# Performance work log

Measured on AMD Instinct MI355X. Metric: run time of the kernel, lower is better.

Reference implementation:

```python
import jax, jax.numpy as jnp
import numpy as np

LATENT_DIM = 64
CONTEXT_DIM = 128
NUM_LAYERS = 5
NUM_BINS = 8
HIDDEN = 256
TAIL_BOUND = 5.0
MIN_BIN_W = 1e-3
MIN_BIN_H = 1e-3
MIN_DERIV = 1e-3
BATCH = 32768


def setup_inputs() -> dict:
    key = jax.random.key(0)
    ks = jax.random.split(key, 8)
    D, C, L, H = LATENT_DIM, CONTEXT_DIM, NUM_LAYERS, HIDDEN
    out_dim = D * (3 * NUM_BINS - 1)  # 64*23 = 1472
    n_tri = D * (D - 1) // 2  # 2016
    s = 0.05
    return {
        "inputs": jax.random.normal(ks[0], (BATCH, D), jnp.float32) * 2.0,
        "context": jax.random.normal(ks[1], (BATCH, C), jnp.float32),
        "W1": jax.random.normal(ks[2], (L, C, H), jnp.float32) * s,
        "b1": jnp.zeros((L, H), jnp.float32),
        "W2": jax.random.normal(ks[3], (L, H, H), jnp.float32) * s,
        "b2": jnp.zeros((L, H), jnp.float32),
        "W3": jax.random.normal(ks[4], (L, H, out_dim), jnp.float32) * s,
        "b3": jnp.zeros((L, out_dim), jnp.float32),
        "lu_bias": jnp.zeros((L, D), jnp.float32),
        "lower_entries": jax.random.normal(ks[5], (L, n_tri), jnp.float32) * s,
        "upper_entries": jax.random.normal(ks[6], (L, n_tri), jnp.float32) * s,
        "upper_diag": jax.random.normal(ks[7], (L, D), jnp.float32) * s,
    }


def _unconstrained_rqs(x, uw, uh, ud):
    """Rational-quadratic spline with linear tails (nflows semantics).
    x: [B, D]; uw/uh: [B, D, NUM_BINS]; ud: [B, D, NUM_BINS-1].
    Returns (y [B,D], logabsdet [B,D])."""
    Bnd = TAIL_BOUND
    nb = NUM_BINS
    inside = (x >= -Bnd) & (x <= Bnd)
    # pad unnormalized derivatives so boundary derivative == 1
    const = float(np.log(np.exp(1.0 - MIN_DERIV) - 1.0))
    ud = jnp.pad(ud, ((0, 0), (0, 0), (1, 1)), constant_values=const)  # [B,D,nb+1]

    w = jax.nn.softmax(uw, axis=-1)
    w = MIN_BIN_W + (1.0 - MIN_BIN_W * nb) * w
    cumw = jnp.concatenate(
        [jnp.zeros(w.shape[:-1] + (1,), w.dtype), jnp.cumsum(w, axis=-1)], axis=-1)
    cumw = 2.0 * Bnd * cumw - Bnd
    cumw = cumw.at[..., 0].set(-Bnd).at[..., -1].set(Bnd)
    widths = cumw[..., 1:] - cumw[..., :-1]

    h = jax.nn.softmax(uh, axis=-1)
    h = MIN_BIN_H + (1.0 - MIN_BIN_H * nb) * h
    cumh = jnp.concatenate(
        [jnp.zeros(h.shape[:-1] + (1,), h.dtype), jnp.cumsum(h, axis=-1)], axis=-1)
    cumh = 2.0 * Bnd * cumh - Bnd
    cumh = cumh.at[..., 0].set(-Bnd).at[..., -1].set(Bnd)
    heights = cumh[..., 1:] - cumh[..., :-1]

    derivs = MIN_DERIV + jax.nn.softplus(ud)  # [B,D,nb+1]
    delta = heights / widths                  # [B,D,nb]

    xc = jnp.clip(x, -Bnd, Bnd)
    # searchsorted: sum(x >= bin_edges) - 1, clipped to valid bin range
    idx = jnp.clip(jnp.sum(xc[..., None] >= cumw, axis=-1) - 1, 0, nb - 1)[..., None]
    g = lambda a: jnp.take_along_axis(a, idx, axis=-1)[..., 0]

    in_cw = g(cumw)
    in_w = g(widths)
    in_ch = g(cumh)
    in_h = g(heights)
    in_delta = g(delta)
    in_d = g(derivs)
    in_d1 = g(derivs[..., 1:])

    theta = (xc - in_cw) / in_w
    tomt = theta * (1.0 - theta)
    numer = in_h * (in_delta * theta * theta + in_d * tomt)
    denom = in_delta + (in_d + in_d1 - 2.0 * in_delta) * tomt
    out = in_ch + numer / denom
    dnum = in_delta * in_delta * (
        in_d1 * theta * theta + 2.0 * in_delta * tomt + in_d * (1.0 - theta) ** 2)
    ld = jnp.log(dnum) - 2.0 * jnp.log(denom)

    return jnp.where(inside, out, x), jnp.where(inside, ld, 0.0)


def _lu_forward(x, lower_e, upper_e, udiag, bias):
    """nflows LULinear: y = L @ (U @ x) + b, logabsdet = sum(log diag(U))."""
    D = x.shape[-1]
    li = jnp.tril_indices(D, -1)
    ui = jnp.triu_indices(D, 1)
    Lm = jnp.eye(D, dtype=x.dtype).at[li].set(lower_e)
    diag = jax.nn.softplus(udiag) + 1e-3
    Um = jnp.zeros((D, D), x.dtype).at[ui].set(upper_e) + jnp.diag(diag)
    y = x @ Um.T
    y = y @ Lm.T + bias
    return y, jnp.sum(jnp.log(diag))


def reference(inputs, context, W1, b1, W2, b2, W3, b3,
              lu_bias, lower_entries, upper_entries, upper_diag):
    x = inputs
    logdet = jnp.zeros(x.shape[0], x.dtype)
    for l in range(NUM_LAYERS):
        # conditioning net (mask=ones => net sees only context)
        hh = jax.nn.relu(context @ W1[l] + b1[l])
        hh = jax.nn.relu(hh @ W2[l] + b2[l])
        params = (hh @ W3[l] + b3[l]).reshape(x.shape[0], LATENT_DIM, 3 * NUM_BINS - 1)
        uw = params[..., :NUM_BINS]
        uh = params[..., NUM_BINS:2 * NUM_BINS]
        ud = params[..., 2 * NUM_BINS:]
        x, ld = _unconstrained_rqs(x, uw, uh, ud)
        logdet = logdet + jnp.sum(ld, axis=-1)
        x, lld = _lu_forward(x, lower_entries[l], upper_entries[l],
                             upper_diag[l], lu_bias[l])
        logdet = logdet + lld
    base = -0.5 * jnp.sum(x * x, axis=-1) - 0.5 * LATENT_DIM * float(np.log(2.0 * np.pi))
    return base + logdet
```

## Files before the change

### kernel.cpp

```cpp
#include <hip/hip_runtime.h>
#include <hip/hip_bf16.h>
#include <math.h>

#define D 64
#define CDIM 128
#define NL 5
#define NB 8
#define HID 256
#define ODIM 1472
#define PPD 23
#define PPDP 24
#define NPAD 1536
#define NTRI 2016
#define BATCH 32768

#define FROWS 64
#define NCH 4
#define CPC 384
#define PPAD 392

typedef unsigned short u16;
typedef __attribute__((ext_vector_type(8))) short bf16x8;
typedef __attribute__((ext_vector_type(8))) unsigned short u16x8;
typedef __attribute__((ext_vector_type(4))) float f32x4;
typedef __attribute__((ext_vector_type(8))) float f32x8;

__device__ __forceinline__ float softplusf(float x) {
    return fmaxf(x, 0.0f) + log1pf(__expf(-fabsf(x)));
}
__device__ __forceinline__ float softplus_fast(float x) {
    return fmaxf(x, 0.0f) + __logf(1.0f + __expf(-fabsf(x)));
}
__device__ __forceinline__ float frcp(float x) { return __builtin_amdgcn_rcpf(x); }
__device__ __forceinline__ u16 f2bf(float f) {
    __hip_bfloat16 h = __float2bfloat16(f);
    return *reinterpret_cast<u16*>(&h);
}
__device__ __forceinline__ float bf2f(u16 u) {
    return __uint_as_float(((unsigned int)u) << 16);
}

__device__ __forceinline__ void gload16(const u16* g, const u16* s) {
    __builtin_amdgcn_global_load_lds(
        (const __attribute__((address_space(1))) unsigned int*)(unsigned long long)(uintptr_t)g,
        (__attribute__((address_space(3))) unsigned int*)(unsigned int)(uintptr_t)s,
        16, 0, 0);
}

__device__ __forceinline__ int xcd_swz(int bid, int nwg) {
    int q = nwg >> 3, r = nwg & 7;
    int xcd = bid & 7, idx = bid >> 3;
    return (xcd < r ? xcd * (q + 1) : r * (q + 1) + (xcd - r) * q) + idx;
}

__global__ void cvt_ctx(const float* __restrict__ c, u16* __restrict__ o) {
    int i = blockIdx.x * 256 + threadIdx.x;
    if (i < BATCH * CDIM) o[i] = f2bf(c[i]);
}

__global__ void prep_w12(const float* __restrict__ W1, const float* __restrict__ W2,
                         u16* __restrict__ W1t, u16* __restrict__ W2t) {
    int i = blockIdx.x * 256 + threadIdx.x;
    if (i < NL * HID * CDIM) {
        int k = i % CDIM; int n = (i / CDIM) % HID; int l = i / (CDIM * HID);
        W1t[i] = f2bf(W1[(l * CDIM + k) * HID + n]);
    }
    if (i < NL * HID * HID) {
        int k = i % HID; int n = (i / HID) % HID; int l = i / (HID * HID);
        W2t[i] = f2bf(W2[(l * HID + k) * HID + n]);
    }
}

__global__ void prep_w3(const float* __restrict__ W3, const float* __restrict__ b3,
                        u16* __restrict__ W3t, float* __restrict__ b3p) {
    int i = blockIdx.x * 256 + threadIdx.x;
    if (i < NL * NPAD * HID) {
        int k = i % HID; int n = (i / HID) % NPAD; int l = i / (HID * NPAD);
        int dd = n / PPDP, p = n % PPDP;
        W3t[i] = (p < PPD) ? f2bf(W3[(l * HID + k) * ODIM + dd * PPD + p]) : (u16)0;
    }
    if (i < NL * NPAD) {
        int n = i % NPAD; int l = i / NPAD;
        int dd = n / PPDP, p = n % PPDP;
        b3p[i] = (p < PPD) ? b3[l * ODIM + dd * PPD + p] : 0.0f;
    }
}

__global__ void lu_prep(const float* __restrict__ lower_e,
                        const float* __restrict__ upper_e,
                        const float* __restrict__ udiag,
                        float* __restrict__ At, float* __restrict__ lu_const) {
    int l = blockIdx.x;
    int t = threadIdx.x;
    __shared__ float Ls[D * D];
    __shared__ float Us[D * D];
    __shared__ float red[4];
    for (int idx = t; idx < D * D; idx += 256) {
        int i = idx >> 6, j = idx & 63;
        float lv;
        if (i == j)      lv = 1.0f;
        else if (i > j)  lv = lower_e[l * NTRI + (i * (i - 1)) / 2 + j];
        else             lv = 0.0f;
        Ls[idx] = lv;
        float uv;
        if (i == j)      uv = softplusf(udiag[l * D + i]) + 0.001f;
        else if (j > i)  uv = upper_e[l * NTRI + i * (D - 1) - (i * (i - 1)) / 2 + (j - i - 1)];
        else             uv = 0.0f;
        Us[idx] = uv;
    }
    __syncthreads();
    for (int idx = t; idx < D * D; idx += 256) {
        int i = idx >> 6, j = idx & 63;
        float acc = 0.0f;
        int km = min(i, j);
        for (int k = 0; k <= km; ++k) acc += Ls[i * D + k] * Us[k * D + j];
        At[(l * D + j) * D + i] = acc;
    }
    if (l == 0) {
        float s = 0.0f;
        for (int i = t; i < NL * D; i += 256)
            s += __logf(softplusf(udiag[i]) + 0.001f);
#pragma unroll
        for (int off = 32; off; off >>= 1) s += __shfl_xor(s, off);
        if ((t & 63) == 0) red[t >> 6] = s;
        __syncthreads();
        if (t == 0) lu_const[0] = red[0] + red[1] + red[2] + red[3];
    }
}

__global__ void init_kernel(const float* __restrict__ inp, float* __restrict__ x,
                            float* __restrict__ logdet) {
    int i = blockIdx.x * 256 + threadIdx.x;
    if (i < BATCH * D) x[i] = inp[i];
    if (i < BATCH) logdet[i] = 0.0f;
}

template<int RELU>
__global__ __launch_bounds__(256) void gemm_bf16(
    const u16* __restrict__ A0, const u16* __restrict__ Bt0,
    const float* __restrict__ bias0, u16* __restrict__ Cv0,
    int N, int K, int ncol, size_t sA, size_t sB, size_t sb, size_t sC)
{
    __shared__ u16 lds[16384];
    const int ly = blockIdx.y;
    const u16* A = A0 + (size_t)ly * sA;
    const u16* Bt = Bt0 + (size_t)ly * sB;
    const float* bias = bias0 + (size_t)ly * sb;
    u16* Cv = Cv0 + (size_t)ly * sC;
    const int t = threadIdx.x;
    const int w = t >> 6, l = t & 63;
    const int wm = w >> 1, wn = w & 1;
    const int wg = xcd_swz(blockIdx.x, gridDim.x);
    const size_t m0 = (size_t)(wg / ncol) * 128;
    const int n0 = (wg % ncol) * 128;
    const int lrow = l & 15, lk = l >> 4;
    const int srow = l >> 3, sslot = l & 7;

    f32x4 acc[4][4] = {};

    for (int k0 = 0; k0 < K; k0 += 64) {
#pragma unroll
        for (int q = 0; q < 4; ++q) {
            int c = q * 4 + w;
            int row = c * 8 + srow;
            int slog = sslot ^ (row & 7);
            gload16(A + (m0 + row) * K + k0 + slog * 8, &lds[c * 512]);
        }
#pragma unroll
        for (int q = 0; q < 4; ++q) {
            int c = q * 4 + w;
            int row = c * 8 + srow;
            int slog = sslot ^ (row & 7);
            gload16(Bt + (size_t)(n0 + row) * K + k0 + slog * 8, &lds[8192 + c * 512]);
        }
        __syncthreads();
#pragma unroll
        for (int ks = 0; ks < 2; ++ks) {
            bf16x8 a[4], b[4];
#pragma unroll
            for (int mf = 0; mf < 4; ++mf) {
                int row = wm * 64 + mf * 16 + lrow;
                int slot = (ks * 4 + lk) ^ (row & 7);
                a[mf] = *(const bf16x8*)&lds[row * 64 + slot * 8];
            }
#pragma unroll
            for (int nf = 0; nf < 4; ++nf) {
                int row = wn * 64 + nf * 16 + lrow;
                int slot = (ks * 4 + lk) ^ (row & 7);
                b[nf] = *(const bf16x8*)&lds[8192 + row * 64 + slot * 8];
            }
#pragma unroll
            for (int mf = 0; mf < 4; ++mf)
#pragma unroll
                for (int nf = 0; nf < 4; ++nf)
                    acc[mf][nf] = __builtin_amdgcn_mfma_f32_16x16x32_bf16(
                        a[mf], b[nf], acc[mf][nf], 0, 0, 0);
        }
        __syncthreads();
    }
#pragma unroll
    for (int nf = 0; nf < 4; ++nf) {
        int col = n0 + wn * 64 + nf * 16 + lrow;
        float bv = bias[col];
#pragma unroll
        for (int mf = 0; mf < 4; ++mf) {
            size_t rbase = m0 + wm * 64 + mf * 16 + lk * 4;
#pragma unroll
            for (int i = 0; i < 4; ++i) {
                float v = acc[mf][nf][i] + bv;
                if (RELU) v = fmaxf(v, 0.0f);
                Cv[(rbase + i) * N + col] = f2bf(v);
            }
        }
    }
}

__device__ __forceinline__ f32x8 cumb(f32x8 p) {
    float m = fmaxf(fmaxf(fmaxf(p[0], p[1]), fmaxf(p[2], p[3])),
                    fmaxf(fmaxf(p[4], p[5]), fmaxf(p[6], p[7])));
    f32x8 e;
    float s = 0.0f;
#pragma unroll
    for (int i = 0; i < 8; ++i) { e[i] = __expf(p[i] - m); s += e[i]; }
    float tt = 0.992f * frcp(s);
    f32x8 c;
    float run = 0.0f;
#pragma unroll
    for (int i = 0; i < 7; ++i) {
        run = fmaf(tt, e[i], run + 0.001f);
        c[i] = fmaf(10.0f, run, -5.0f);
    }
    c[7] = 5.0f;
    return c;
}

__device__ __forceinline__ void rqs_v(float xv, f32x8 uw, f32x8 uh, f32x8 ud,
                                      float& yo, float& ldo) {
    f32x8 cw = cumb(uw);
    f32x8 ch = cumb(uh);
    f32x8 dv;
#pragma unroll
    for (int i = 0; i < 7; ++i) dv[i] = 0.001f + softplus_fast(ud[i]);
    float xc = fminf(fmaxf(xv, -5.0f), 5.0f);
    float icw = -5.0f, icw1 = cw[0], ich = -5.0f, ich1 = ch[0];
    float d0 = 1.0f, d1 = dv[0];
#pragma unroll
    for (int k = 1; k < 8; ++k) {
        bool sel = (xc >= cw[k - 1]);
        icw  = sel ? cw[k - 1] : icw;
        icw1 = sel ? cw[k]     : icw1;
        ich  = sel ? ch[k - 1] : ich;
        ich1 = sel ? ch[k]     : ich1;
        d0   = sel ? dv[k - 1] : d0;
        d1   = sel ? ((k < 7) ? dv[k] : 1.0f) : d1;
    }
    float iw  = icw1 - icw;
    float ih  = ich1 - ich;
    float riw = frcp(iw);
    float dlt = ih * riw;
    float th  = (xc - icw) * riw;
    float omt = 1.0f - th;
    float tomt = th * omt;
    float numer = ih * (dlt * th * th + d0 * tomt);
    float den = dlt + (d0 + d1 - 2.0f * dlt) * tomt;
    float rden = frcp(den);
    float outv = ich + numer * rden;
    float dnum = dlt * dlt * (d1 * th * th + 2.0f * dlt * tomt + d0 * omt * omt);
    float ld = __logf(dnum * rden * rden);
    bool inside = (xv >= -5.0f) && (xv <= 5.0f);
    yo  = inside ? outv : xv;
    ldo = inside ? ld : 0.0f;
}

__global__ __launch_bounds__(512, 2) void gemm3_spline_lu(
    const u16* __restrict__ hh2,
    const u16* __restrict__ W3t,
    const float* __restrict__ b3p,
    const float* __restrict__ At, const float* __restrict__ lu_bias,
    float* __restrict__ x, float* __restrict__ logdet, int lay)
{
    __shared__ u16 hh2_s[FROWS * 256];
    __shared__ u16 params_s[FROWS * PPAD];
    __shared__ float y_s[FROWS * 65];
    __shared__ float ld_s[FROWS];
    const int t = threadIdx.x;
    const int w = t >> 6, ln = t & 63;
    const int lr = ln & 15, lk = ln >> 4;
    const int rbase = blockIdx.x * FROWS;

#pragma unroll
    for (int r = 0; r < 4; ++r) {
        int basec = (r * 8 + w) * 64;
        int c = basec + ln;
        int row = c >> 5, rem = c & 31;
        int kb = rem >> 3, sl = rem & 7;
        gload16(hh2 + (size_t)(rbase + row) * HID + kb * 64 + (sl ^ (row & 7)) * 8,
                &hh2_s[basec * 8]);
    }
    if (t < FROWS) ld_s[t] = 0.0f;
    __syncthreads();

    float ld_acc = 0.0f;
    const int srow = t & 63, sd0 = t >> 6;

    for (int ch = 0; ch < NCH; ++ch) {
        float xv0 = x[(size_t)(rbase + srow) * D + ch * 16 + sd0];
        float xv1 = x[(size_t)(rbase + srow) * D + ch * 16 + sd0 + 8];

        f32x4 acc[3][4] = {};
        const u16* wb = W3t + (size_t)(ch * CPC + w * 48 + lr) * HID + lk * 8;
#pragma unroll
        for (int ks = 0; ks < 8; ++ks) {
            bf16x8 hf[4];
#pragma unroll
            for (int rf = 0; rf < 4; ++rf) {
                int row = rf * 16 + lr;
                hf[rf] = *(const bf16x8*)&hh2_s[row * 256 + (ks >> 1) * 64
                              + ((((ks & 1) * 4) + lk) ^ (lr & 7)) * 8];
            }
#pragma unroll
            for (int mf = 0; mf < 3; ++mf) {
                bf16x8 wf = *(const bf16x8*)(wb + (size_t)mf * 16 * HID + ks * 32);
#pragma unroll
                for (int rf = 0; rf < 4; ++rf)
                    acc[mf][rf] = __builtin_amdgcn_mfma_f32_16x16x32_bf16(
                        wf, hf[rf], acc[mf][rf], 0, 0, 0);
            }
        }
        __syncthreads();

        {
            const float* bb = b3p + ch * CPC + w * 48 + 4 * lk;
#pragma unroll
            for (int mf = 0; mf < 3; ++mf) {
                float4 bv = *(const float4*)(bb + mf * 16);
#pragma unroll
                for (int rf = 0; rf < 4; ++rf) {
                    f32x4 v = acc[mf][rf];
                    unsigned int lo = (unsigned int)f2bf(v[0] + bv.x)
                                    | ((unsigned int)f2bf(v[1] + bv.y) << 16);
                    unsigned int hi = (unsigned int)f2bf(v[2] + bv.z)
                                    | ((unsigned int)f2bf(v[3] + bv.w) << 16);
                    uint2 pv; pv.x = lo; pv.y = hi;
                    int r = rf * 16 + lr;
                    int cbase = w * 48 + mf * 16 + 4 * lk;
                    *(uint2*)&params_s[r * PPAD + cbase] = pv;
                }
            }
        }
        __syncthreads();

#pragma unroll
        for (int pr = 0; pr < 2; ++pr) {
            int dg = ch * 16 + sd0 + pr * 8;
            const u16x8* pp = (const u16x8*)&params_s[srow * PPAD + (sd0 + pr * 8) * PPDP];
            u16x8 q0 = pp[0], q1 = pp[1], q2 = pp[2];
            f32x8 uw, uh, ud;
#pragma unroll
            for (int j = 0; j < 8; ++j) {
                uw[j] = bf2f(q0[j]);
                uh[j] = bf2f(q1[j]);
                ud[j] = bf2f(q2[j]);
            }
            float xv = pr ? xv1 : xv0;
            float y, ldv;
            rqs_v(xv, uw, uh, ud, y, ldv);
            y_s[srow * 65 + dg] = y;
            ld_acc += ldv;
        }
    }

    atomicAdd(&ld_s[srow], ld_acc);
    __syncthreads();
    if (t < FROWS) logdet[rbase + t] += ld_s[t];

#pragma unroll
    for (int p = 0; p < 8; ++p) {
        int idx = p * 512 + t;
        int r = idx >> 6, i = idx & 63;
        float acc2 = lu_bias[lay * D + i];
        const float* ap = At + (size_t)lay * D * D + i;
#pragma unroll 8
        for (int j = 0; j < D; ++j)
            acc2 = fmaf(y_s[r * 65 + j], ap[j * D], acc2);
        x[(size_t)(rbase + r) * D + i] = acc2;
    }
}

__global__ void final_kernel(const float* __restrict__ x,
                             const float* __restrict__ logdet,
                             const float* __restrict__ lu_const,
                             float* __restrict__ out) {
    int t = threadIdx.x;
    int b = blockIdx.x * 4 + (t >> 6);
    int d = t & 63;
    float v = x[(size_t)b * D + d];
    float s = v * v;
#pragma unroll
    for (int off = 32; off; off >>= 1) s += __shfl_xor(s, off);
    if (d == 0)
        out[b] = logdet[b] + lu_const[0] - 0.5f * s - 0.5f * 64.0f * 1.8378770664093453f;
}

extern "C" void kernel_launch(void* const* d_in, const int* in_sizes, int n_in,
                              void* d_out, int out_size, void* d_ws, size_t ws_size,
                              hipStream_t stream) {
    const float* inputs  = (const float*)d_in[0];
    const float* context = (const float*)d_in[1];
    const float* W1      = (const float*)d_in[2];
    const float* b1      = (const float*)d_in[3];
    const float* W2      = (const float*)d_in[4];
    const float* b2      = (const float*)d_in[5];
    const float* W3      = (const float*)d_in[6];
    const float* b3      = (const float*)d_in[7];
    const float* lu_bias = (const float*)d_in[8];
    const float* lower_e = (const float*)d_in[9];
    const float* upper_e = (const float*)d_in[10];
    const float* udiag   = (const float*)d_in[11];
    float* out = (float*)d_out;

    char* p = (char*)d_ws;
    auto alloc = [&](size_t bytes) { void* r = p; p += (bytes + 255) & ~(size_t)255; return r; };
    float* x        = (float*)alloc((size_t)BATCH * D * 4);
    float* logdet   = (float*)alloc((size_t)BATCH * 4);
    float* At       = (float*)alloc((size_t)NL * D * D * 4);
    float* lu_const = (float*)alloc(256);
    u16*   ctx_bf   = (u16*)alloc((size_t)BATCH * CDIM * 2);
    u16*   hh1      = (u16*)alloc((size_t)NL * BATCH * HID * 2);
    u16*   hh2      = (u16*)alloc((size_t)NL * BATCH * HID * 2);
    u16*   W1t      = (u16*)alloc((size_t)NL * HID * CDIM * 2);
    u16*   W2t      = (u16*)alloc((size_t)NL * HID * HID * 2);
    u16*   W3t      = (u16*)alloc((size_t)NL * NPAD * HID * 2);
    float* b3p      = (float*)alloc((size_t)NL * NPAD * 4);

    cvt_ctx<<<(BATCH * CDIM + 255) / 256, 256, 0, stream>>>(context, ctx_bf);
    prep_w12<<<(NL * HID * HID + 255) / 256, 256, 0, stream>>>(W1, W2, W1t, W2t);
    prep_w3<<<(NL * NPAD * HID + 255) / 256, 256, 0, stream>>>(W3, b3, W3t, b3p);
    lu_prep<<<NL, 256, 0, stream>>>(lower_e, upper_e, udiag, At, lu_const);
    init_kernel<<<(BATCH * D + 255) / 256, 256, 0, stream>>>(inputs, x, logdet);

    dim3 gmlp((BATCH / 128) * 2, NL);
    gemm_bf16<1><<<gmlp, 256, 0, stream>>>(
        ctx_bf, W1t, b1, hh1, HID, CDIM, 2,
        0, (size_t)HID * CDIM, HID, (size_t)BATCH * HID);
    gemm_bf16<1><<<gmlp, 256, 0, stream>>>(
        hh1, W2t, b2, hh2, HID, HID, 2,
        (size_t)BATCH * HID, (size_t)HID * HID, HID, (size_t)BATCH * HID);

    for (int lay = 0; lay < NL; ++lay) {
        gemm3_spline_lu<<<BATCH / FROWS, 512, 0, stream>>>(
            hh2 + (size_t)lay * BATCH * HID,
            W3t + (size_t)lay * NPAD * HID, b3p + (size_t)lay * NPAD,
            At, lu_bias, x, logdet, lay);
    }
    final_kernel<<<BATCH / 4, 256, 0, stream>>>(x, logdet, lu_const, out);
}
```

Before: 588.0 us.

## Split GEMM3 into smaller chunks, raise occupancy, swizzle params LDS, reuse LU weights

Halves the per-chunk output width (8 chunks of 192 columns) and splits the 8 waves as 4 column groups by 2 row groups, so each wave holds a 3x2 accumulator set instead of 3x4. This cuts register pressure and allows launch bounds of 4 blocks per CU. The params LDS buffer shrinks and uses an XOR swizzle instead of padding to avoid bank conflicts. The LU matvec now reuses each At element across 8 rows per thread. The costs are more chunk iterations and barriers, plus lower MFMA reuse of the loaded W3 fragments.

```diff
diff --git a/kernel.cpp b/kernel.cpp
--- a/kernel.cpp
+++ b/kernel.cpp
@@ -15,9 +15,9 @@
 #define BATCH 32768
 
 #define FROWS 64
-#define NCH 4
-#define CPC 384
-#define PPAD 392
+#define NCH 8
+#define CPC 192
+#define PROWB 384
 
 typedef unsigned short u16;
 typedef __attribute__((ext_vector_type(8))) short bf16x8;
@@ -272,7 +272,7 @@
     ldo = inside ? ld : 0.0f;
 }
 
-__global__ __launch_bounds__(512, 2) void gemm3_spline_lu(
+__global__ __launch_bounds__(512, 4) void gemm3_spline_lu(
     const u16* __restrict__ hh2,
     const u16* __restrict__ W3t,
     const float* __restrict__ b3p,
@@ -280,12 +280,13 @@
     float* __restrict__ x, float* __restrict__ logdet, int lay)
 {
     __shared__ u16 hh2_s[FROWS * 256];
-    __shared__ u16 params_s[FROWS * PPAD];
+    __shared__ u16 params_s[FROWS * CPC];
     __shared__ float y_s[FROWS * 65];
     __shared__ float ld_s[FROWS];
     const int t = threadIdx.x;
     const int w = t >> 6, ln = t & 63;
     const int lr = ln & 15, lk = ln >> 4;
+    const int wc = w & 3, wr = w >> 2;
     const int rbase = blockIdx.x * FROWS;
 
 #pragma unroll
@@ -301,20 +302,19 @@
     __syncthreads();
 
     float ld_acc = 0.0f;
-    const int srow = t & 63, sd0 = t >> 6;
+    const int srow = ln, sd = w;
 
     for (int ch = 0; ch < NCH; ++ch) {
-        float xv0 = x[(size_t)(rbase + srow) * D + ch * 16 + sd0];
-        float xv1 = x[(size_t)(rbase + srow) * D + ch * 16 + sd0 + 8];
-
-        f32x4 acc[3][4] = {};
-        const u16* wb = W3t + (size_t)(ch * CPC + w * 48 + lr) * HID + lk * 8;
+        float xv = x[(size_t)(rbase + srow) * D + ch * 8 + sd];
+
+        f32x4 acc[3][2] = {};
+        const u16* wb = W3t + (size_t)(ch * CPC + wc * 48 + lr) * HID + lk * 8;
 #pragma unroll
         for (int ks = 0; ks < 8; ++ks) {
-            bf16x8 hf[4];
-#pragma unroll
-            for (int rf = 0; rf < 4; ++rf) {
-                int row = rf * 16 + lr;
+            bf16x8 hf[2];
+#pragma unroll
+            for (int rf = 0; rf < 2; ++rf) {
+                int row = wr * 32 + rf * 16 + lr;
                 hf[rf] = *(const bf16x8*)&hh2_s[row * 256 + (ks >> 1) * 64
                               + ((((ks & 1) * 4) + lk) ^ (lr & 7)) * 8];
             }
@@ -322,7 +322,7 @@
             for (int mf = 0; mf < 3; ++mf) {
                 bf16x8 wf = *(const bf16x8*)(wb + (size_t)mf * 16 * HID + ks * 32);
 #pragma unroll
-                for (int rf = 0; rf < 4; ++rf)
+                for (int rf = 0; rf < 2; ++rf)
                     acc[mf][rf] = __builtin_amdgcn_mfma_f32_16x16x32_bf16(
                         wf, hf[rf], acc[mf][rf], 0, 0, 0);
             }
@@ -330,31 +330,33 @@
         __syncthreads();
 
         {
-            const float* bb = b3p + ch * CPC + w * 48 + 4 * lk;
+            const float* bb = b3p + ch * CPC + wc * 48 + 4 * lk;
 #pragma unroll
             for (int mf = 0; mf < 3; ++mf) {
                 float4 bv = *(const float4*)(bb + mf * 16);
 #pragma unroll
-                for (int rf = 0; rf < 4; ++rf) {
+                for (int rf = 0; rf < 2; ++rf) {
                     f32x4 v = acc[mf][rf];
                     unsigned int lo = (unsigned int)f2bf(v[0] + bv.x)
                                     | ((unsigned int)f2bf(v[1] + bv.y) << 16);
                     unsigned int hi = (unsigned int)f2bf(v[2] + bv.z)
                                     | ((unsigned int)f2bf(v[3] + bv.w) << 16);
                     uint2 pv; pv.x = lo; pv.y = hi;
-                    int r = rf * 16 + lr;
-                    int cbase = w * 48 + mf * 16 + 4 * lk;
-                    *(uint2*)&params_s[r * PPAD + cbase] = pv;
+                    int r = wr * 32 + rf * 16 + lr;
+                    int slot = wc * 6 + mf * 2 + (lk >> 1);
+                    int boff = r * PROWB + (((slot ^ (r & 7)) << 4) | ((lk & 1) << 3));
+                    *(uint2*)((char*)params_s + boff) = pv;
                 }
             }
         }
         __syncthreads();
 
-#pragma unroll
-        for (int pr = 0; pr < 2; ++pr) {
-            int dg = ch * 16 + sd0 + pr * 8;
-            const u16x8* pp = (const u16x8*)&params_s[srow * PPAD + (sd0 + pr * 8) * PPDP];
-            u16x8 q0 = pp[0], q1 = pp[1], q2 = pp[2];
+        {
+            int base = srow * PROWB;
+            int s0 = 3 * sd, rx = srow & 7;
+            u16x8 q0 = *(const u16x8*)((const char*)params_s + base + (((s0 + 0) ^ rx) << 4));
+            u16x8 q1 = *(const u16x8*)((const char*)params_s + base + (((s0 + 1) ^ rx) << 4));
+            u16x8 q2 = *(const u16x8*)((const char*)params_s + base + (((s0 + 2) ^ rx) << 4));
             f32x8 uw, uh, ud;
 #pragma unroll
             for (int j = 0; j < 8; ++j) {
@@ -362,10 +364,9 @@
                 uh[j] = bf2f(q1[j]);
                 ud[j] = bf2f(q2[j]);
             }
-            float xv = pr ? xv1 : xv0;
             float y, ldv;
             rqs_v(xv, uw, uh, ud, y, ldv);
-            y_s[srow * 65 + dg] = y;
+            y_s[srow * 65 + ch * 8 + sd] = y;
             ld_acc += ldv;
         }
     }
@@ -374,16 +375,22 @@
     __syncthreads();
     if (t < FROWS) logdet[rbase + t] += ld_s[t];
 
-#pragma unroll
-    for (int p = 0; p < 8; ++p) {
-        int idx = p * 512 + t;
-        int r = idx >> 6, i = idx & 63;
-        float acc2 = lu_bias[lay * D + i];
-        const float* ap = At + (size_t)lay * D * D + i;
+    {
+        float acc2[8];
+        float bv = lu_bias[lay * D + ln];
+#pragma unroll
+        for (int p = 0; p < 8; ++p) acc2[p] = bv;
+        const float* ap = At + (size_t)lay * D * D + ln;
 #pragma unroll 8
-        for (int j = 0; j < D; ++j)
-            acc2 = fmaf(y_s[r * 65 + j], ap[j * D], acc2);
-        x[(size_t)(rbase + r) * D + i] = acc2;
+        for (int j = 0; j < D; ++j) {
+            float aj = ap[j * D];
+#pragma unroll
+            for (int p = 0; p < 8; ++p)
+                acc2[p] = fmaf(y_s[(w * 8 + p) * 65 + j], aj, acc2[p]);
+        }
+#pragma unroll
+        for (int p = 0; p < 8; ++p)
+            x[(size_t)(rbase + w * 8 + p) * D + ln] = acc2[p];
     }
 }
 
```

Result: slower. 655.8 us (+11.5%).
